# Performance work log

Hardware: AMD Instinct MI355X
Metric: run time of the kernel (lower is better)

Reference implementation:

```python
import jax, jax.numpy as jnp
import numpy as np

C_RATIO, T_RATIO = 0.8, 0.9

def _mlp(v, w1, w2):
    # v: [b, n]; w1: [hid, n]; w2: [n, hid]  (1x1x1 convs on pooled vector == matmuls)
    return jnp.einsum('nh,bh->bn', w2, jax.nn.relu(jnp.einsum('hn,bn->bh', w1, v)))

def _wta(x, ratio):
    # winner-take-all along last dim: keep top ceil(ratio*n) entries, zero the rest
    k = int(np.ceil(ratio * x.shape[-1]))
    thr = jax.lax.top_k(x, k)[0][..., -1:]
    mask = (x >= thr).astype(x.dtype)
    return x * mask, mask

def setup_inputs() -> dict:
    key = jax.random.key(0)
    ks = jax.random.split(key, 5)
    b, f, c, h, w = 16, 8, 256, 32, 32
    x = jax.random.normal(ks[0], (b, f, c, h, w), jnp.float32)
    ta_w1 = jax.random.normal(ks[1], (f, f), jnp.float32) * 0.3   # TimeAttention conv1 (reduction=1)
    ta_w2 = jax.random.normal(ks[2], (f, f), jnp.float32) * 0.3   # TimeAttention conv2
    ca_w1 = jax.random.normal(ks[3], (c, c), jnp.float32) * 0.06  # ChannelAttention conv1
    ca_w2 = jax.random.normal(ks[4], (c, c), jnp.float32) * 0.06  # ChannelAttention conv2
    return {"x": x, "ta_w1": ta_w1, "ta_w2": ta_w2, "ca_w1": ca_w1, "ca_w2": ca_w2}

def reference(x, ta_w1, ta_w2, ca_w1, ca_w2):
    # TimeAttention: global avg/max pool over (c,h,w) -> [b,f], shared MLP, sigmoid
    t_avg = x.mean(axis=(2, 3, 4))
    t_max = x.max(axis=(2, 3, 4))
    ta = jax.nn.sigmoid(_mlp(t_avg, ta_w1, ta_w2) + _mlp(t_max, ta_w1, ta_w2))  # [b,f]
    out = x * ta[:, :, None, None, None]
    # ChannelAttention on ta*x: pool over (f,h,w) -> [b,c]
    c_avg = out.mean(axis=(1, 3, 4))
    c_max = out.max(axis=(1, 3, 4))
    ca = jax.nn.sigmoid(_mlp(c_avg, ca_w1, ca_w2) + _mlp(c_max, ca_w1, ca_w2))  # [b,c]
    # winner-take-all saliency masking
    sal_c, mask_c = _wta(ca, C_RATIO)   # [b,c]
    sal_t, mask_t = _wta(ta, T_RATIO)   # [b,f]
    coef = (sal_t[:, :, None] * sal_c[:, None, :])[..., None, None]   # [b,f,c,1,1]
    mask = (mask_t[:, :, None] * mask_c[:, None, :])[..., None, None]
    return x * mask * coef
```

## Files before the change

kernel.cpp:

```cpp
#include <hip/hip_runtime.h>
#include <math.h>

#define B 16
#define F 8
#define C 256
#define HW 1024
#define NROWS (B*F*C)
#define KC 205

typedef float f4 __attribute__((ext_vector_type(4)));

__global__ __launch_bounds__(256) void k_rowstat(const float* __restrict__ x,
                                                 float* __restrict__ sums,
                                                 float* __restrict__ maxs) {
    const int wave = threadIdx.x >> 6;
    const int lane = threadIdx.x & 63;
    const int row0 = blockIdx.x * 8 + wave * 2;
    const float* p0 = x + (size_t)row0 * HW + lane * 4;
    const float* p1 = p0 + HW;

    float4 a0 = *reinterpret_cast<const float4*>(p0);
    float4 a1 = *reinterpret_cast<const float4*>(p0 + 256);
    float4 a2 = *reinterpret_cast<const float4*>(p0 + 512);
    float4 a3 = *reinterpret_cast<const float4*>(p0 + 768);
    float4 b0 = *reinterpret_cast<const float4*>(p1);
    float4 b1 = *reinterpret_cast<const float4*>(p1 + 256);
    float4 b2 = *reinterpret_cast<const float4*>(p1 + 512);
    float4 b3 = *reinterpret_cast<const float4*>(p1 + 768);

    float s0 = (((a0.x + a0.y) + (a0.z + a0.w)) + ((a1.x + a1.y) + (a1.z + a1.w)))
             + (((a2.x + a2.y) + (a2.z + a2.w)) + ((a3.x + a3.y) + (a3.z + a3.w)));
    float m0 = fmaxf(fmaxf(fmaxf(fmaxf(a0.x, a0.y), fmaxf(a0.z, a0.w)),
                           fmaxf(fmaxf(a1.x, a1.y), fmaxf(a1.z, a1.w))),
                     fmaxf(fmaxf(fmaxf(a2.x, a2.y), fmaxf(a2.z, a2.w)),
                           fmaxf(fmaxf(a3.x, a3.y), fmaxf(a3.z, a3.w))));
    float s1 = (((b0.x + b0.y) + (b0.z + b0.w)) + ((b1.x + b1.y) + (b1.z + b1.w)))
             + (((b2.x + b2.y) + (b2.z + b2.w)) + ((b3.x + b3.y) + (b3.z + b3.w)));
    float m1 = fmaxf(fmaxf(fmaxf(fmaxf(b0.x, b0.y), fmaxf(b0.z, b0.w)),
                           fmaxf(fmaxf(b1.x, b1.y), fmaxf(b1.z, b1.w))),
                     fmaxf(fmaxf(fmaxf(b2.x, b2.y), fmaxf(b2.z, b2.w)),
                           fmaxf(fmaxf(b3.x, b3.y), fmaxf(b3.z, b3.w))));

#pragma unroll
    for (int off = 32; off > 0; off >>= 1) {
        s0 += __shfl_down(s0, off);
        m0 = fmaxf(m0, __shfl_down(m0, off));
        s1 += __shfl_down(s1, off);
        m1 = fmaxf(m1, __shfl_down(m1, off));
    }
    if (lane == 0) {
        sums[row0] = s0; maxs[row0] = m0;
        sums[row0 + 1] = s1; maxs[row0 + 1] = m1;
    }
}

__global__ __launch_bounds__(256) void k_att(const float* __restrict__ sums,
                                             const float* __restrict__ maxs,
                                             const float* __restrict__ tw1,
                                             const float* __restrict__ tw2,
                                             const float* __restrict__ w1,
                                             const float* __restrict__ w2,
                                             float* __restrict__ srow) {
    __shared__ float tavg[F], tmx[F], th[F], ta_s[F];
    __shared__ float vavg[C], vmax[C], hsum[C], ca[C];
    const int b    = blockIdx.x;
    const int t    = threadIdx.x;
    const int wave = t >> 6;
    const int lane = t & 63;

    for (int f = wave; f < F; f += 4) {
        const float* sp = sums + (b * F + f) * C;
        const float* mp = maxs + (b * F + f) * C;
        float s = (sp[lane] + sp[lane + 64]) + (sp[lane + 128] + sp[lane + 192]);
        float m = fmaxf(fmaxf(mp[lane], mp[lane + 64]),
                        fmaxf(mp[lane + 128], mp[lane + 192]));
#pragma unroll
        for (int off = 32; off > 0; off >>= 1) {
            s += __shfl_down(s, off);
            m = fmaxf(m, __shfl_down(m, off));
        }
        if (lane == 0) { tavg[f] = s * (1.f / (float)(C * HW)); tmx[f] = m; }
    }
    __syncthreads();

    if (t < F) {
        float ha = 0.f, hm = 0.f;
        for (int n = 0; n < F; ++n) {
            float w = tw1[t * F + n];
            ha += w * tavg[n];
            hm += w * tmx[n];
        }
        th[t] = fmaxf(ha, 0.f) + fmaxf(hm, 0.f);
    }
    __syncthreads();
    if (t < F) {
        float o = 0.f;
        for (int h = 0; h < F; ++h) o += tw2[t * F + h] * th[h];
        ta_s[t] = 1.f / (1.f + expf(-o));
    }
    __syncthreads();

    {
        float s = 0.f, m = -INFINITY;
        for (int f = 0; f < F; ++f) {
            float w = ta_s[f];
            s += w * sums[(b * F + f) * C + t];
            m = fmaxf(m, w * maxs[(b * F + f) * C + t]);
        }
        vavg[t] = s * (1.f / (float)(F * HW));
        vmax[t] = m;
    }
    __syncthreads();

    {
        float ha = 0.f, hm = 0.f;
        const float4* w1r = reinterpret_cast<const float4*>(w1 + t * C);
        for (int n = 0; n < C / 4; ++n) {
            float4 w = w1r[n];
            ha += w.x * vavg[n*4] + w.y * vavg[n*4+1] + w.z * vavg[n*4+2] + w.w * vavg[n*4+3];
            hm += w.x * vmax[n*4] + w.y * vmax[n*4+1] + w.z * vmax[n*4+2] + w.w * vmax[n*4+3];
        }
        hsum[t] = fmaxf(ha, 0.f) + fmaxf(hm, 0.f);
    }
    __syncthreads();

    float cav;
    {
        float o = 0.f;
        const float4* w2r = reinterpret_cast<const float4*>(w2 + t * C);
        for (int h = 0; h < C / 4; ++h) {
            float4 w = w2r[h];
            o += w.x * hsum[h*4] + w.y * hsum[h*4+1] + w.z * hsum[h*4+2] + w.w * hsum[h*4+3];
        }
        cav = 1.f / (1.f + expf(-o));
        ca[t] = cav;
    }
    __syncthreads();

    int rank = 0;
    for (int j = 0; j < C; ++j) rank += (ca[j] > cav);
    float sc = (rank < KC) ? cav : 0.f;
    for (int f = 0; f < F; ++f)
        srow[b * (F * C) + f * C + t] = ta_s[f] * sc;
}

__global__ __launch_bounds__(256) void k_scale(const float* __restrict__ x,
                                               const float* __restrict__ srow,
                                               float* __restrict__ out) {
    const int t    = threadIdx.x;
    const int row0 = blockIdx.x * 16;
    const f4* x4 = reinterpret_cast<const f4*>(x);
    f4* o4 = reinterpret_cast<f4*>(out);

    float sc[16];
#pragma unroll
    for (int i = 0; i < 16; ++i) sc[i] = srow[row0 + i];

#pragma unroll
    for (int g = 0; g < 4; ++g) {
        const size_t base = (size_t)(row0 + g * 4) * 256 + t;
        const float s0 = sc[g*4], s1 = sc[g*4+1], s2 = sc[g*4+2], s3 = sc[g*4+3];
        const f4 z = {0.f, 0.f, 0.f, 0.f};
        f4 v0 = z, v1 = z, v2 = z, v3 = z;
        if (s0 != 0.f) v0 = x4[base];
        if (s1 != 0.f) v1 = x4[base + 256];
        if (s2 != 0.f) v2 = x4[base + 512];
        if (s3 != 0.f) v3 = x4[base + 768];
        v0 *= s0; v1 *= s1; v2 *= s2; v3 *= s3;
        o4[base]       = v0;
        o4[base + 256] = v1;
        o4[base + 512] = v2;
        o4[base + 768] = v3;
    }
}

extern "C" void kernel_launch(void* const* d_in, const int* in_sizes, int n_in,
                              void* d_out, int out_size, void* d_ws, size_t ws_size,
                              hipStream_t stream) {
    const float* x     = (const float*)d_in[0];
    const float* ta_w1 = (const float*)d_in[1];
    const float* ta_w2 = (const float*)d_in[2];
    const float* ca_w1 = (const float*)d_in[3];
    const float* ca_w2 = (const float*)d_in[4];
    float* out = (float*)d_out;

    float* ws   = (float*)d_ws;
    float* sums = ws;
    float* maxs = ws + NROWS;
    float* srow = ws + 2 * NROWS;

    k_rowstat<<<NROWS / 8, 256, 0, stream>>>(x, sums, maxs);
    k_att<<<B, 256, 0, stream>>>(sums, maxs, ta_w1, ta_w2, ca_w1, ca_w2, srow);
    k_scale<<<2048, 256, 0, stream>>>(x, srow, out);
}
```

Before: 82.34 us.

## Split attention kernel work across 1024 threads per batch with partial reductions

The attention kernel now runs with 1024 threads per block instead of 256. Each channel's f-pooling, both 256x256 matvecs and the rank counting are split four ways over quarters of the reduction dimension, then combined through shared-memory partial sums. The aim is to shorten the serial per-thread loops in this 16-block latency-bound kernel. The cost is extra barriers and shared-memory traffic.

```diff
diff --git a/kernel.cpp b/kernel.cpp
--- a/kernel.cpp
+++ b/kernel.cpp
@@ -54,23 +54,26 @@
     }
 }
 
-__global__ __launch_bounds__(256) void k_att(const float* __restrict__ sums,
-                                             const float* __restrict__ maxs,
-                                             const float* __restrict__ tw1,
-                                             const float* __restrict__ tw2,
-                                             const float* __restrict__ w1,
-                                             const float* __restrict__ w2,
-                                             float* __restrict__ srow) {
+__global__ __launch_bounds__(1024) void k_att(const float* __restrict__ sums,
+                                              const float* __restrict__ maxs,
+                                              const float* __restrict__ tw1,
+                                              const float* __restrict__ tw2,
+                                              const float* __restrict__ w1,
+                                              const float* __restrict__ w2,
+                                              float* __restrict__ srow) {
     __shared__ float tavg[F], tmx[F], th[F], ta_s[F];
     __shared__ float vavg[C], vmax[C], hsum[C], ca[C];
+    __shared__ float pa[4][C], pm[4][C];
     const int b    = blockIdx.x;
     const int t    = threadIdx.x;
     const int wave = t >> 6;
     const int lane = t & 63;
-
-    for (int f = wave; f < F; f += 4) {
-        const float* sp = sums + (b * F + f) * C;
-        const float* mp = maxs + (b * F + f) * C;
+    const int c    = t & 255;
+    const int q    = t >> 8;
+
+    if (wave < F) {
+        const float* sp = sums + (b * F + wave) * C;
+        const float* mp = maxs + (b * F + wave) * C;
         float s = (sp[lane] + sp[lane + 64]) + (sp[lane + 128] + sp[lane + 192]);
         float m = fmaxf(fmaxf(mp[lane], mp[lane + 64]),
                         fmaxf(mp[lane + 128], mp[lane + 192]));
@@ -79,7 +82,7 @@
             s += __shfl_down(s, off);
             m = fmaxf(m, __shfl_down(m, off));
         }
-        if (lane == 0) { tavg[f] = s * (1.f / (float)(C * HW)); tmx[f] = m; }
+        if (lane == 0) { tavg[wave] = s * (1.f / (float)(C * HW)); tmx[wave] = m; }
     }
     __syncthreads();
 
@@ -101,47 +104,79 @@
     __syncthreads();
 
     {
-        float s = 0.f, m = -INFINITY;
-        for (int f = 0; f < F; ++f) {
-            float w = ta_s[f];
-            s += w * sums[(b * F + f) * C + t];
-            m = fmaxf(m, w * maxs[(b * F + f) * C + t]);
-        }
-        vavg[t] = s * (1.f / (float)(F * HW));
-        vmax[t] = m;
+        const int f0 = 2 * q, f1 = 2 * q + 1;
+        const float wa = ta_s[f0], wb = ta_s[f1];
+        float sA = wa * sums[(b * F + f0) * C + c] + wb * sums[(b * F + f1) * C + c];
+        float mA = fmaxf(wa * maxs[(b * F + f0) * C + c],
+                         wb * maxs[(b * F + f1) * C + c]);
+        pa[q][c] = sA; pm[q][c] = mA;
+    }
+    __syncthreads();
+    if (q == 0) {
+        vavg[c] = ((pa[0][c] + pa[1][c]) + (pa[2][c] + pa[3][c])) * (1.f / (float)(F * HW));
+        vmax[c] = fmaxf(fmaxf(pm[0][c], pm[1][c]), fmaxf(pm[2][c], pm[3][c]));
     }
     __syncthreads();
 
     {
         float ha = 0.f, hm = 0.f;
-        const float4* w1r = reinterpret_cast<const float4*>(w1 + t * C);
-        for (int n = 0; n < C / 4; ++n) {
+        const float4* w1r = reinterpret_cast<const float4*>(w1 + c * C) + q * 16;
+        const int n0 = q * 64;
+#pragma unroll
+        for (int n = 0; n < 16; ++n) {
             float4 w = w1r[n];
-            ha += w.x * vavg[n*4] + w.y * vavg[n*4+1] + w.z * vavg[n*4+2] + w.w * vavg[n*4+3];
-            hm += w.x * vmax[n*4] + w.y * vmax[n*4+1] + w.z * vmax[n*4+2] + w.w * vmax[n*4+3];
-        }
-        hsum[t] = fmaxf(ha, 0.f) + fmaxf(hm, 0.f);
-    }
-    __syncthreads();
-
-    float cav;
+            const int nn = n0 + n * 4;
+            ha += w.x * vavg[nn] + w.y * vavg[nn+1] + w.z * vavg[nn+2] + w.w * vavg[nn+3];
+            hm += w.x * vmax[nn] + w.y * vmax[nn+1] + w.z * vmax[nn+2] + w.w * vmax[nn+3];
+        }
+        pa[q][c] = ha; pm[q][c] = hm;
+    }
+    __syncthreads();
+    if (q == 0) {
+        float ha = (pa[0][c] + pa[1][c]) + (pa[2][c] + pa[3][c]);
+        float hm = (pm[0][c] + pm[1][c]) + (pm[2][c] + pm[3][c]);
+        hsum[c] = fmaxf(ha, 0.f) + fmaxf(hm, 0.f);
+    }
+    __syncthreads();
+
     {
         float o = 0.f;
-        const float4* w2r = reinterpret_cast<const float4*>(w2 + t * C);
-        for (int h = 0; h < C / 4; ++h) {
+        const float4* w2r = reinterpret_cast<const float4*>(w2 + c * C) + q * 16;
+        const int h0 = q * 64;
+#pragma unroll
+        for (int h = 0; h < 16; ++h) {
             float4 w = w2r[h];
-            o += w.x * hsum[h*4] + w.y * hsum[h*4+1] + w.z * hsum[h*4+2] + w.w * hsum[h*4+3];
-        }
-        cav = 1.f / (1.f + expf(-o));
-        ca[t] = cav;
-    }
-    __syncthreads();
-
-    int rank = 0;
-    for (int j = 0; j < C; ++j) rank += (ca[j] > cav);
-    float sc = (rank < KC) ? cav : 0.f;
-    for (int f = 0; f < F; ++f)
-        srow[b * (F * C) + f * C + t] = ta_s[f] * sc;
+            const int hh = h0 + h * 4;
+            o += w.x * hsum[hh] + w.y * hsum[hh+1] + w.z * hsum[hh+2] + w.w * hsum[hh+3];
+        }
+        pa[q][c] = o;
+    }
+    __syncthreads();
+    if (q == 0) {
+        float o = (pa[0][c] + pa[1][c]) + (pa[2][c] + pa[3][c]);
+        ca[c] = 1.f / (1.f + expf(-o));
+    }
+    __syncthreads();
+
+    {
+        const float cav = ca[c];
+        int cnt = 0;
+        const int j0 = q * 64;
+        for (int j = 0; j < 64; ++j) cnt += (ca[j0 + j] > cav);
+        pm[q][c] = (float)cnt;
+    }
+    __syncthreads();
+    if (q == 0) {
+        int rank = (int)(((pm[0][c] + pm[1][c]) + (pm[2][c] + pm[3][c])));
+        vavg[c] = (rank < KC) ? ca[c] : 0.f;
+    }
+    __syncthreads();
+
+    {
+        const float scv = vavg[c];
+        srow[b * (F * C) + q * C + c]       = ta_s[q] * scv;
+        srow[b * (F * C) + (q + 4) * C + c] = ta_s[q + 4] * scv;
+    }
 }
 
 __global__ __launch_bounds__(256) void k_scale(const float* __restrict__ x,
@@ -190,6 +225,6 @@
     float* srow = ws + 2 * NROWS;
 
     k_rowstat<<<NROWS / 8, 256, 0, stream>>>(x, sums, maxs);
-    k_att<<<B, 256, 0, stream>>>(sums, maxs, ta_w1, ta_w2, ca_w1, ca_w2, srow);
+    k_att<<<B, 1024, 0, stream>>>(sums, maxs, ta_w1, ta_w2, ca_w1, ca_w2, srow);
     k_scale<<<2048, 256, 0, stream>>>(x, srow, out);
 }
```

Measured after the change: 81.19 us. Within noise of the previous version (-1.4%).

## Split attention MLP across more blocks and move top-k ranking into scale kernel

Applied to the files above, without the earlier changes.

The single-kernel attention stage ran on only 16 blocks (one per batch), serializing two 256x256 matvecs per block. It is now split into two kernels with 256 blocks each, where each wave computes dot products via coalesced float4 loads and shuffle reductions. The rank-based winner-take-all and the ta*ca coefficient product move into the scale kernel, which recomputes ranks per block from shared memory. This adds an extra launch and redundant per-block rank work, and the time-attention part is recomputed in all 16 blocks per batch.

```diff
diff --git a/kernel.cpp b/kernel.cpp
--- a/kernel.cpp
+++ b/kernel.cpp
@@ -54,19 +54,17 @@
     }
 }
 
-__global__ __launch_bounds__(256) void k_att(const float* __restrict__ sums,
-                                             const float* __restrict__ maxs,
-                                             const float* __restrict__ tw1,
-                                             const float* __restrict__ tw2,
-                                             const float* __restrict__ w1,
-                                             const float* __restrict__ w2,
-                                             float* __restrict__ srow) {
+__global__ __launch_bounds__(256) void k_l1(const float* __restrict__ sums,
+                                            const float* __restrict__ maxs,
+                                            const float* __restrict__ tw1,
+                                            const float* __restrict__ tw2,
+                                            const float* __restrict__ w1,
+                                            float* __restrict__ ta_g,
+                                            float* __restrict__ hsum_g) {
     __shared__ float tavg[F], tmx[F], th[F], ta_s[F];
-    __shared__ float vavg[C], vmax[C], hsum[C], ca[C];
-    const int b    = blockIdx.x;
-    const int t    = threadIdx.x;
-    const int wave = t >> 6;
-    const int lane = t & 63;
+    __shared__ __align__(16) float vavg[C], vmax[C];
+    const int b = blockIdx.x >> 4, g = blockIdx.x & 15;
+    const int t = threadIdx.x, wave = t >> 6, lane = t & 63;
 
     for (int f = wave; f < F; f += 4) {
         const float* sp = sums + (b * F + f) * C;
@@ -99,6 +97,7 @@
         ta_s[t] = 1.f / (1.f + expf(-o));
     }
     __syncthreads();
+    if (g == 0 && t < F) ta_g[b * F + t] = ta_s[t];
 
     {
         float s = 0.f, m = -INFINITY;
@@ -112,54 +111,83 @@
     }
     __syncthreads();
 
+    const float4 va = reinterpret_cast<const float4*>(vavg)[lane];
+    const float4 vm = reinterpret_cast<const float4*>(vmax)[lane];
+#pragma unroll
+    for (int k = 0; k < 4; ++k) {
+        const int h = 16 * g + wave * 4 + k;
+        float4 w = reinterpret_cast<const float4*>(w1 + h * C)[lane];
+        float ha = (w.x * va.x + w.y * va.y) + (w.z * va.z + w.w * va.w);
+        float hm = (w.x * vm.x + w.y * vm.y) + (w.z * vm.z + w.w * vm.w);
+#pragma unroll
+        for (int off = 32; off > 0; off >>= 1) {
+            ha += __shfl_down(ha, off);
+            hm += __shfl_down(hm, off);
+        }
+        if (lane == 0) hsum_g[b * C + h] = fmaxf(ha, 0.f) + fmaxf(hm, 0.f);
+    }
+}
+
+__global__ __launch_bounds__(256) void k_l2(const float* __restrict__ hsum_g,
+                                            const float* __restrict__ w2,
+                                            float* __restrict__ ca_g) {
+    __shared__ __align__(16) float hs[C];
+    const int b = blockIdx.x >> 4, g = blockIdx.x & 15;
+    const int t = threadIdx.x, wave = t >> 6, lane = t & 63;
+
+    hs[t] = hsum_g[b * C + t];
+    __syncthreads();
+    const float4 hv = reinterpret_cast<const float4*>(hs)[lane];
+#pragma unroll
+    for (int k = 0; k < 4; ++k) {
+        const int c = 16 * g + wave * 4 + k;
+        float4 w = reinterpret_cast<const float4*>(w2 + c * C)[lane];
+        float o = (w.x * hv.x + w.y * hv.y) + (w.z * hv.z + w.w * hv.w);
+#pragma unroll
+        for (int off = 32; off > 0; off >>= 1) o += __shfl_down(o, off);
+        if (lane == 0) ca_g[b * C + c] = 1.f / (1.f + expf(-o));
+    }
+}
+
+__global__ __launch_bounds__(256) void k_scale(const float* __restrict__ x,
+                                               const float* __restrict__ ta_g,
+                                               const float* __restrict__ ca_g,
+                                               float* __restrict__ out) {
+    __shared__ float ca[C];
+    __shared__ float pcnt[16][16];
+    __shared__ float srow_s[16];
+    const int b = blockIdx.x >> 7, chunk = blockIdx.x & 127;
+    const int t = threadIdx.x;
+    const int f = chunk >> 4, c0 = (chunk & 15) * 16;
+
+    ca[t] = ca_g[b * C + t];
+    __syncthreads();
+
     {
-        float ha = 0.f, hm = 0.f;
-        const float4* w1r = reinterpret_cast<const float4*>(w1 + t * C);
-        for (int n = 0; n < C / 4; ++n) {
-            float4 w = w1r[n];
-            ha += w.x * vavg[n*4] + w.y * vavg[n*4+1] + w.z * vavg[n*4+2] + w.w * vavg[n*4+3];
-            hm += w.x * vmax[n*4] + w.y * vmax[n*4+1] + w.z * vmax[n*4+2] + w.w * vmax[n*4+3];
-        }
-        hsum[t] = fmaxf(ha, 0.f) + fmaxf(hm, 0.f);
-    }
-    __syncthreads();
-
-    float cav;
-    {
-        float o = 0.f;
-        const float4* w2r = reinterpret_cast<const float4*>(w2 + t * C);
-        for (int h = 0; h < C / 4; ++h) {
-            float4 w = w2r[h];
-            o += w.x * hsum[h*4] + w.y * hsum[h*4+1] + w.z * hsum[h*4+2] + w.w * hsum[h*4+3];
-        }
-        cav = 1.f / (1.f + expf(-o));
-        ca[t] = cav;
-    }
-    __syncthreads();
-
-    int rank = 0;
-    for (int j = 0; j < C; ++j) rank += (ca[j] > cav);
-    float sc = (rank < KC) ? cav : 0.f;
-    for (int f = 0; f < F; ++f)
-        srow[b * (F * C) + f * C + t] = ta_s[f] * sc;
-}
-
-__global__ __launch_bounds__(256) void k_scale(const float* __restrict__ x,
-                                               const float* __restrict__ srow,
-                                               float* __restrict__ out) {
-    const int t    = threadIdx.x;
+        const int ch = t >> 4, seg = t & 15;
+        const float cav = ca[c0 + ch];
+        int cnt = 0;
+#pragma unroll
+        for (int jj = 0; jj < 16; ++jj) cnt += (ca[seg * 16 + jj] > cav);
+        pcnt[ch][seg] = (float)cnt;
+    }
+    __syncthreads();
+    if (t < 16) {
+        float r = 0.f;
+#pragma unroll
+        for (int s = 0; s < 16; ++s) r += pcnt[t][s];
+        srow_s[t] = (((int)r) < KC) ? ta_g[b * F + f] * ca[c0 + t] : 0.f;
+    }
+    __syncthreads();
+
     const int row0 = blockIdx.x * 16;
     const f4* x4 = reinterpret_cast<const f4*>(x);
     f4* o4 = reinterpret_cast<f4*>(out);
-
-    float sc[16];
-#pragma unroll
-    for (int i = 0; i < 16; ++i) sc[i] = srow[row0 + i];
-
 #pragma unroll
     for (int g = 0; g < 4; ++g) {
         const size_t base = (size_t)(row0 + g * 4) * 256 + t;
-        const float s0 = sc[g*4], s1 = sc[g*4+1], s2 = sc[g*4+2], s3 = sc[g*4+3];
+        const float s0 = srow_s[g*4], s1 = srow_s[g*4+1];
+        const float s2 = srow_s[g*4+2], s3 = srow_s[g*4+3];
         const f4 z = {0.f, 0.f, 0.f, 0.f};
         f4 v0 = z, v1 = z, v2 = z, v3 = z;
         if (s0 != 0.f) v0 = x4[base];
@@ -184,12 +212,15 @@
     const float* ca_w2 = (const float*)d_in[4];
     float* out = (float*)d_out;
 
-    float* ws   = (float*)d_ws;
-    float* sums = ws;
-    float* maxs = ws + NROWS;
-    float* srow = ws + 2 * NROWS;
+    float* ws     = (float*)d_ws;
+    float* sums   = ws;
+    float* maxs   = ws + NROWS;
+    float* ta_g   = ws + 2 * NROWS;
+    float* hsum_g = ws + 2 * NROWS + 128;
+    float* ca_g   = ws + 2 * NROWS + 128 + B * C;
 
     k_rowstat<<<NROWS / 8, 256, 0, stream>>>(x, sums, maxs);
-    k_att<<<B, 256, 0, stream>>>(sums, maxs, ta_w1, ta_w2, ca_w1, ca_w2, srow);
-    k_scale<<<2048, 256, 0, stream>>>(x, srow, out);
-}
+    k_l1<<<B * 16, 256, 0, stream>>>(sums, maxs, ta_w1, ta_w2, ca_w1, ta_g, hsum_g);
+    k_l2<<<B * 16, 256, 0, stream>>>(hsum_g, ca_w2, ca_g);
+    k_scale<<<2048, 256, 0, stream>>>(x, ta_g, ca_g, out);
+}
```

Measured after the change: 71.66 us. 13.0% less time.
